# Optimization experiments

Hardware: AMD Instinct MI355X
Metric: run time of the kernel (lower is better)

Reference implementation:

```python
import jax, jax.numpy as jnp
import numpy as np

SEQ, BATCH, D_IN, D_HID, D_OUT = 2048, 256, 512, 512, 1000


def setup_inputs() -> dict:
    key = jax.random.key(0)
    ks = jax.random.split(key, 15)
    s_in = 1.0 / np.sqrt(D_IN)
    s_h = 1.0 / np.sqrt(D_HID)
    def lin(k, fan_in, shape, scale):
        return jax.random.uniform(k, shape, jnp.float32, -scale, scale)
    return {
        "x": jax.random.normal(ks[0], (SEQ, BATCH, D_IN), jnp.float32),
        # weights stored as [in, out] so y = x @ W + b
        "Wz": lin(ks[1], D_IN, (D_IN, D_HID), s_in),  "bz": lin(ks[2], D_IN, (D_HID,), s_in),
        "Uz": lin(ks[3], D_HID, (D_HID, D_HID), s_h), "buz": lin(ks[4], D_HID, (D_HID,), s_h),
        "Wr": lin(ks[5], D_IN, (D_IN, D_HID), s_in),  "br": lin(ks[6], D_IN, (D_HID,), s_in),
        "Ur": lin(ks[7], D_HID, (D_HID, D_HID), s_h), "bur": lin(ks[8], D_HID, (D_HID,), s_h),
        "Wh": lin(ks[9], D_IN, (D_IN, D_HID), s_in),  "bh": lin(ks[10], D_IN, (D_HID,), s_in),
        "Uh": lin(ks[11], D_HID, (D_HID, D_HID), s_h), "buh": lin(ks[12], D_HID, (D_HID,), s_h),
        "Wfc": lin(ks[13], D_HID, (D_HID, D_OUT), s_h), "bfc": lin(ks[14], D_HID, (D_OUT,), s_h),
    }


def reference(x, Wz, bz, Uz, buz, Wr, br, Ur, bur, Wh, bh, Uh, buh, Wfc, bfc):
    B, H = x.shape[1], Uz.shape[0]

    def gru_step(h, xt):
        # xt: [B, D_IN], h: [B, H]
        z = jax.nn.sigmoid(xt @ Wz + bz + h @ Uz + buz)
        r = jax.nn.sigmoid(xt @ Wr + br + h @ Ur + bur)
        h_tild = jnp.tanh(xt @ Wh + bh + (r * h) @ Uh + buh)
        h_new = (1.0 - z) * h + z * h_tild
        return h_new, None

    h0 = jnp.zeros((B, H), x.dtype)  # zero init hidden (broadcast-equivalent)
    h, _ = jax.lax.scan(gru_step, h0, x)
    out = jax.nn.relu(h) @ Wfc + bfc        # [B, D_OUT]
    out = out[None]                          # [1, B, D_OUT]
    return jax.nn.log_softmax(out, axis=1)  # dim=1 as in torch module
```

## Files before the change

kernel.cpp:

```cpp
#include <hip/hip_runtime.h>


typedef unsigned short ushort_t;
typedef unsigned int uint_t;
typedef __bf16 bf16_t;
typedef bf16_t bf16x8 __attribute__((ext_vector_type(8)));
typedef float f32x4 __attribute__((ext_vector_type(4)));
typedef uint_t u32x4 __attribute__((ext_vector_type(4)));

__device__ __forceinline__ ushort_t f2bf(float f) {
  uint_t u = __float_as_uint(f);
  u += 0x7FFFu + ((u >> 16) & 1u);
  return (ushort_t)(u >> 16);
}
__device__ __forceinline__ float bfu2f(uint_t h) { return __uint_as_float(h << 16); }

__device__ __forceinline__ uint_t atom_add_ret(uint_t* p, uint_t v) {
  uint_t old;
  asm volatile("global_atomic_add %0, %1, %2, off sc0\n\t"
               "s_waitcnt vmcnt(0)"
               : "=v"(old) : "v"(p), "v"(v) : "memory");
  return old;
}
__device__ __forceinline__ void atom_add_noret(uint_t* p, uint_t v) {
  asm volatile("global_atomic_add %0, %1, off" :: "v"(p), "v"(v) : "memory");
}

__global__ __launch_bounds__(256) void prep_kernel(
    const float* __restrict__ Wz, const float* __restrict__ Wr, const float* __restrict__ Wh,
    const float* __restrict__ Uz, const float* __restrict__ Ur, const float* __restrict__ Uh,
    const float* __restrict__ bz, const float* __restrict__ buz,
    const float* __restrict__ br, const float* __restrict__ bur,
    const float* __restrict__ bh, const float* __restrict__ buh,
    ushort_t* __restrict__ UT, ushort_t* __restrict__ WT, float* __restrict__ gbias)
{
  const int idx = blockIdx.x * 256 + threadIdx.x;
  {
    const int gate = idx >> 18, n = (idx >> 9) & 511, k = idx & 511;
    const float* U = (gate == 0) ? Uz : (gate == 1 ? Ur : Uh);
    UT[idx] = f2bf(U[k * 512 + n]);
  }
  {
    const int n = idx >> 9, k = idx & 511;
    const int gate = n >> 9, nn = n & 511;
    const float* W = (gate == 0) ? Wz : (gate == 1 ? Wr : Wh);
    WT[idx] = f2bf(W[k * 512 + nn]);
  }
  if (idx < 1536) {
    const int gate = idx >> 9, nn = idx & 511;
    gbias[idx] = (gate == 0) ? (bz[nn] + buz[nn])
               : (gate == 1) ? (br[nn] + bur[nn])
                             : (bh[nn] + buh[nn]);
  }
}

__global__ __launch_bounds__(256) void gate_gemm(
    const float* __restrict__ x,
    const ushort_t* __restrict__ WT,
    const float* __restrict__ gbias,
    ushort_t* __restrict__ gout,
    int mtiles)
{
  __shared__ ushort_t A_sh[128 * 72];
  __shared__ ushort_t B_sh[128 * 72];
  const int bid = blockIdx.x;
  int mt, nt;
  if ((mtiles & 31) == 0) {
    const int sb = bid / 384;
    const int r = bid - sb * 384;
    mt = sb * 32 + (r & 31);
    nt = r >> 5;
  } else {
    mt = bid / 12;
    nt = bid - mt * 12;
  }
  const int mrow0 = mt * 128;
  const int ncol0 = nt * 128;
  const int tid = threadIdx.x;
  const int wid = tid >> 6;
  const int lane = tid & 63;
  const int wm = wid >> 1, wn = wid & 1;
  const int l15 = lane & 15, l4 = lane >> 4;

  const f32x4 vzero = {0.f, 0.f, 0.f, 0.f};
  f32x4 acc[4][4];
#pragma unroll
  for (int m = 0; m < 4; ++m)
#pragma unroll
    for (int n = 0; n < 4; ++n) acc[m][n] = vzero;

  const int ar = tid >> 4, ak = tid & 15;
  const int bn = tid >> 3, bk = tid & 7;

  for (int ks = 0; ks < 8; ++ks) {
    if (ks) __syncthreads();
    const int k0 = ks * 64;
#pragma unroll
    for (int p = 0; p < 8; ++p) {
      const int r = p * 16 + ar;
      const float4 v = *(const float4*)&x[(size_t)(mrow0 + r) * 512 + (k0 + ak * 4)];
      ushort4 hv;
      hv.x = f2bf(v.x); hv.y = f2bf(v.y); hv.z = f2bf(v.z); hv.w = f2bf(v.w);
      *(ushort4*)&A_sh[r * 72 + ak * 4] = hv;
    }
#pragma unroll
    for (int p = 0; p < 4; ++p) {
      const int n = p * 32 + bn;
      *(uint4*)&B_sh[n * 72 + bk * 8] =
          *(const uint4*)&WT[(size_t)(ncol0 + n) * 512 + (k0 + bk * 8)];
    }
    __syncthreads();
#pragma unroll
    for (int kk = 0; kk < 2; ++kk) {
      bf16x8 a[4], b[4];
#pragma unroll
      for (int m = 0; m < 4; ++m)
        a[m] = *(const bf16x8*)&A_sh[(wm * 64 + m * 16 + l15) * 72 + kk * 32 + l4 * 8];
#pragma unroll
      for (int n = 0; n < 4; ++n)
        b[n] = *(const bf16x8*)&B_sh[(wn * 64 + n * 16 + l15) * 72 + kk * 32 + l4 * 8];
#pragma unroll
      for (int m = 0; m < 4; ++m)
#pragma unroll
        for (int n = 0; n < 4; ++n)
          acc[m][n] = __builtin_amdgcn_mfma_f32_16x16x32_bf16(a[m], b[n], acc[m][n], 0, 0, 0);
    }
  }
#pragma unroll
  for (int n = 0; n < 4; ++n) {
    const int gcol = ncol0 + wn * 64 + n * 16 + l15;
    const float bv = gbias[gcol];
#pragma unroll
    for (int m = 0; m < 4; ++m) {
      const int grow = mrow0 + wm * 64 + m * 16 + l4 * 4;
#pragma unroll
      for (int q = 0; q < 4; ++q)
        gout[(size_t)(grow + q) * 1536 + gcol] = f2bf(acc[m][n][q] + bv);
    }
  }
}

__device__ __forceinline__ bool flag_barrier(uint_t* gflags, int j, int lane, int wid, int tid,
                                             uint_t nbar, int* s_dead) {
  asm volatile("s_waitcnt vmcnt(0)" ::: "memory");
  __syncthreads();
  if (tid == 0) atom_add_noret(gflags + j * 16, 1u);
  if (wid == 0) {
    int cnt = 0;
    for (;;) {
      uint_t v = nbar;
      if (lane < 16) v = atom_add_ret(gflags + lane * 16, 0u);
      if (!__any(v < nbar)) break;
      if (++cnt > (1 << 15)) { *s_dead = 1; break; }
    }
  }
  __syncthreads();
  return *s_dead != 0;
}

__device__ __forceinline__ void stage16x512(const ushort_t* __restrict__ src, int g,
                                            ushort_t* dst_lds, int tid) {
  const ushort_t* p[4];
#pragma unroll
  for (int k = 0; k < 4; ++k) {
    const int idx = tid + (k << 8);
    const int r = idx >> 6, kc = idx & 63;
    p[k] = src + (((g * 16 + r) << 9) + kc * 8);
  }
  u32x4 v0, v1, v2, v3;
  asm volatile(
      "global_load_dwordx4 %0, %4, off sc0\n\t"
      "global_load_dwordx4 %1, %5, off sc0\n\t"
      "global_load_dwordx4 %2, %6, off sc0\n\t"
      "global_load_dwordx4 %3, %7, off sc0\n\t"
      "s_waitcnt vmcnt(0)"
      : "=&v"(v0), "=&v"(v1), "=&v"(v2), "=&v"(v3)
      : "v"(p[0]), "v"(p[1]), "v"(p[2]), "v"(p[3])
      : "memory");
#pragma unroll
  for (int k = 0; k < 4; ++k) {
    const int idx = tid + (k << 8);
    const int r = idx >> 6, kc = idx & 63;
    *(u32x4*)&dst_lds[r * 520 + kc * 8] = (k == 0) ? v0 : (k == 1) ? v1 : (k == 2) ? v2 : v3;
  }
}

__global__ __launch_bounds__(256, 1) void gru_rec(
    const ushort_t* __restrict__ UT,
    const ushort_t* __restrict__ gates,
    ushort_t* __restrict__ h_buf,
    ushort_t* __restrict__ rh_buf,
    float* __restrict__ h_state,
    uint_t* __restrict__ bars,
    int Tc, int first)
{
  __shared__ ushort_t h_st[16 * 520];
  __shared__ float z_sh[512];
  __shared__ float hown[512];
  __shared__ float red[512];
  __shared__ int s_dead;

  const int tid = threadIdx.x;
  const int bid = blockIdx.x;
  const int g = bid & 15;
  const int j = bid >> 4;
  const int wid = tid >> 6;
  const int lane = tid & 63;
  const int l15 = lane & 15;
  const int l4 = lane >> 4;
  if (tid == 0) s_dead = 0;

  uint_t* gflags = bars + g * 256;
  uint_t nbar = 0;

  const int p1gate = wid >> 1;
  const int p1nt = wid & 1;
  const int p2nt = wid >> 1;
  const int p2kh = wid & 1;

  bf16x8 UB[16];
  {
    const size_t base = (size_t)((p1gate << 9) + j * 32 + p1nt * 16 + l15) * 512 + (size_t)(l4 * 8);
#pragma unroll
    for (int kk = 0; kk < 16; ++kk) UB[kk] = *(const bf16x8*)&UT[base + (size_t)kk * 32];
  }
  bf16x8 UH[8];
  {
    const size_t base = (size_t)(1024 + j * 32 + p2nt * 16 + l15) * 512 + (size_t)(p2kh * 256 + l4 * 8);
#pragma unroll
    for (int kk = 0; kk < 8; ++kk) UH[kk] = *(const bf16x8*)&UT[base + (size_t)kk * 32];
  }

  if (first) {
    for (int i = tid; i < 512; i += 256) {
      const int r = i >> 5, c = i & 31;
      h_buf[((g * 16 + r) << 9) + j * 32 + c] = 0;
      hown[i] = 0.f;
    }
  } else {
    for (int i = tid; i < 512; i += 256) {
      const int r = i >> 5, c = i & 31;
      hown[i] = h_state[((g * 16 + r) << 9) + j * 32 + c];
    }
  }
  ++nbar;
  if (flag_barrier(gflags, j, lane, wid, tid, nbar, &s_dead)) return;

  const int colg1 = j * 32 + p1nt * 16 + l15;
  const int colg2 = j * 32 + p2nt * 16 + l15;

  uint_t c1u[4], c2u[4], n1u[4], n2u[4];
  {
    const size_t gb = (size_t)(g * 16) * 1536;
#pragma unroll
    for (int q = 0; q < 4; ++q) {
      n1u[q] = gates[gb + (size_t)(l4 * 4 + q) * 1536 + (p1gate << 9) + colg1];
      n2u[q] = gates[gb + (size_t)(l4 * 4 + q) * 1536 + 1024 + colg2];
    }
  }

  for (int tt = 0; tt < Tc; ++tt) {
    stage16x512(h_buf, g, h_st, tid);
    __syncthreads();
#pragma unroll
    for (int q = 0; q < 4; ++q) { c1u[q] = n1u[q]; c2u[q] = n2u[q]; }
    {
      const ushort_t* ap = &h_st[l15 * 520 + l4 * 8];
      f32x4 a0 = {0.f, 0.f, 0.f, 0.f}, a1 = {0.f, 0.f, 0.f, 0.f};
#pragma unroll
      for (int kk = 0; kk < 16; kk += 2) {
        a0 = __builtin_amdgcn_mfma_f32_16x16x32_bf16(*(const bf16x8*)(ap + kk * 32), UB[kk], a0, 0, 0, 0);
        a1 = __builtin_amdgcn_mfma_f32_16x16x32_bf16(*(const bf16x8*)(ap + kk * 32 + 32), UB[kk + 1], a1, 0, 0, 0);
      }
      const f32x4 acc = a0 + a1;
      const int lc = p1nt * 16 + l15;
#pragma unroll
      for (int q = 0; q < 4; ++q) {
        const int row = l4 * 4 + q;
        const float pre = acc[q] + bfu2f(c1u[q]);
        const float s = 1.f / (1.f + __expf(-pre));
        if (p1gate == 0) z_sh[row * 32 + lc] = s;
        else rh_buf[((g * 16 + row) << 9) + j * 32 + lc] = f2bf(s * hown[row * 32 + lc]);
      }
    }
    ++nbar;
    if (flag_barrier(gflags, j, lane, wid, tid, nbar, &s_dead)) break;

    stage16x512(rh_buf, g, h_st, tid);
    __syncthreads();
    if (tt + 1 < Tc) {
      const size_t gb = (size_t)((size_t)(tt + 1) * 256 + g * 16) * 1536;
#pragma unroll
      for (int q = 0; q < 4; ++q) {
        n1u[q] = gates[gb + (size_t)(l4 * 4 + q) * 1536 + (p1gate << 9) + colg1];
        n2u[q] = gates[gb + (size_t)(l4 * 4 + q) * 1536 + 1024 + colg2];
      }
    }
    {
      const ushort_t* ap = &h_st[l15 * 520 + p2kh * 256 + l4 * 8];
      f32x4 a0 = {0.f, 0.f, 0.f, 0.f}, a1 = {0.f, 0.f, 0.f, 0.f};
#pragma unroll
      for (int kk = 0; kk < 8; kk += 2) {
        a0 = __builtin_amdgcn_mfma_f32_16x16x32_bf16(*(const bf16x8*)(ap + kk * 32), UH[kk], a0, 0, 0, 0);
        a1 = __builtin_amdgcn_mfma_f32_16x16x32_bf16(*(const bf16x8*)(ap + kk * 32 + 32), UH[kk + 1], a1, 0, 0, 0);
      }
      const f32x4 acc = a0 + a1;
      if (p2kh == 1) {
#pragma unroll
        for (int q = 0; q < 4; ++q) red[p2nt * 256 + (l4 * 4 + q) * 16 + l15] = acc[q];
      }
      __syncthreads();
      if (p2kh == 0) {
        const int lc = p2nt * 16 + l15;
#pragma unroll
        for (int q = 0; q < 4; ++q) {
          const int row = l4 * 4 + q;
          const float dot = acc[q] + red[p2nt * 256 + row * 16 + l15];
          float pre = dot + bfu2f(c2u[q]);
          pre = fminf(15.f, fmaxf(-15.f, pre));
          const float e = __expf(2.f * pre);
          const float th = (e - 1.f) / (e + 1.f);
          const float z = z_sh[row * 32 + lc];
          const float hold = hown[row * 32 + lc];
          const float hnew = (1.f - z) * hold + z * th;
          hown[row * 32 + lc] = hnew;
          h_buf[((g * 16 + row) << 9) + j * 32 + lc] = f2bf(hnew);
          if (tt == Tc - 1) h_state[((g * 16 + row) << 9) + j * 32 + lc] = hnew;
        }
      }
    }
    ++nbar;
    if (flag_barrier(gflags, j, lane, wid, tid, nbar, &s_dead)) break;
  }
}

__global__ __launch_bounds__(256) void fc_kernel(
    const float* __restrict__ h, const float* __restrict__ Wfc,
    const float* __restrict__ bfc, float* __restrict__ logits)
{
  __shared__ float hsh[16][520];
  const int tid = threadIdx.x;
  const int by = blockIdx.y;
  {
    const int r = tid >> 4, seg = tid & 15;
    const float* src = &h[(size_t)(by * 16 + r) * 512 + seg * 32];
#pragma unroll
    for (int i = 0; i < 8; ++i) {
      float4 v = *(const float4*)&src[i * 4];
      v.x = fmaxf(v.x, 0.f); v.y = fmaxf(v.y, 0.f);
      v.z = fmaxf(v.z, 0.f); v.w = fmaxf(v.w, 0.f);
      *(float4*)&hsh[r][seg * 32 + i * 4] = v;
    }
  }
  __syncthreads();
  const int c = tid & 63, rq = tid >> 6;
  const int gc = blockIdx.x * 64 + c;
  if (gc >= 1000) return;
  float acc0 = 0.f, acc1 = 0.f, acc2 = 0.f, acc3 = 0.f;
  for (int k = 0; k < 512; ++k) {
    const float w = Wfc[(size_t)k * 1000 + gc];
    acc0 += hsh[rq * 4 + 0][k] * w;
    acc1 += hsh[rq * 4 + 1][k] * w;
    acc2 += hsh[rq * 4 + 2][k] * w;
    acc3 += hsh[rq * 4 + 3][k] * w;
  }
  const float bv = bfc[gc];
  const int r0 = by * 16 + rq * 4;
  logits[(size_t)(r0 + 0) * 1000 + gc] = acc0 + bv;
  logits[(size_t)(r0 + 1) * 1000 + gc] = acc1 + bv;
  logits[(size_t)(r0 + 2) * 1000 + gc] = acc2 + bv;
  logits[(size_t)(r0 + 3) * 1000 + gc] = acc3 + bv;
}

__global__ __launch_bounds__(256) void lsm_kernel(const float* __restrict__ logits,
                                                  float* __restrict__ out)
{
  const int c = blockIdx.x, tid = threadIdx.x;
  const int wid = tid >> 6, lane = tid & 63;
  __shared__ float red[8];
  const float v = logits[(size_t)tid * 1000 + c];
  float m = v;
#pragma unroll
  for (int o = 32; o >= 1; o >>= 1) m = fmaxf(m, __shfl_xor(m, o));
  if (lane == 0) red[wid] = m;
  __syncthreads();
  m = fmaxf(fmaxf(red[0], red[1]), fmaxf(red[2], red[3]));
  float s = __expf(v - m);
#pragma unroll
  for (int o = 32; o >= 1; o >>= 1) s += __shfl_xor(s, o);
  if (lane == 0) red[4 + wid] = s;
  __syncthreads();
  s = red[4] + red[5] + red[6] + red[7];
  out[(size_t)tid * 1000 + c] = (v - m) - __logf(s);
}

extern "C" void kernel_launch(void* const* d_in, const int* in_sizes, int n_in,
                              void* d_out, int out_size, void* d_ws, size_t ws_size,
                              hipStream_t stream) {
  (void)in_sizes; (void)n_in; (void)out_size;
  const float* x   = (const float*)d_in[0];
  const float* Wz  = (const float*)d_in[1];
  const float* bz  = (const float*)d_in[2];
  const float* Uz  = (const float*)d_in[3];
  const float* buz = (const float*)d_in[4];
  const float* Wr  = (const float*)d_in[5];
  const float* br  = (const float*)d_in[6];
  const float* Ur  = (const float*)d_in[7];
  const float* bur = (const float*)d_in[8];
  const float* Wh  = (const float*)d_in[9];
  const float* bh  = (const float*)d_in[10];
  const float* Uh  = (const float*)d_in[11];
  const float* buh = (const float*)d_in[12];
  const float* Wfc = (const float*)d_in[13];
  const float* bfc = (const float*)d_in[14];
  float* out = (float*)d_out;
  char* ws = (char*)d_ws;

  ushort_t* UT     = (ushort_t*)(ws + 0);
  ushort_t* WT     = (ushort_t*)(ws + 1572864);
  float*    gbias  = (float*)(ws + 3145728);
  ushort_t* h_buf  = (ushort_t*)(ws + 3151872);
  ushort_t* rh_buf = (ushort_t*)(ws + 3414016);
  float*    hstate = (float*)(ws + 3676160);
  float*    logits = (float*)(ws + 4200448);
  uint_t*   bars   = (uint_t*)(ws + 5224448);
  ushort_t* gates  = (ushort_t*)(ws + 5240832);

  const size_t fixed = 5240832;
  const size_t per_step = (size_t)256 * 1536 * 2;
  int Tc_max = 2048;
  if (ws_size < fixed + (size_t)2048 * per_step) {
    const size_t avail = (ws_size > fixed) ? (ws_size - fixed) : 0;
    Tc_max = (int)(avail / per_step);
    Tc_max &= ~15;
    if (Tc_max < 16) Tc_max = 16;
  }

  prep_kernel<<<3072, 256, 0, stream>>>(Wz, Wr, Wh, Uz, Ur, Uh,
                                        bz, buz, br, bur, bh, buh, UT, WT, gbias);

  int done = 0;
  while (done < 2048) {
    const int Tc = (2048 - done < Tc_max) ? (2048 - done) : Tc_max;
    const int mtiles = Tc * 2;
    gate_gemm<<<mtiles * 12, 256, 0, stream>>>(x + (size_t)done * 256 * 512, WT, gbias, gates, mtiles);
    hipMemsetAsync(bars, 0, 16384, stream);
    gru_rec<<<256, 256, 0, stream>>>(UT, gates, h_buf, rh_buf, hstate, bars, Tc, done == 0 ? 1 : 0);
    done += Tc;
  }
  fc_kernel<<<dim3(16, 16), 256, 0, stream>>>(hstate, Wfc, bfc, logits);
  lsm_kernel<<<1000, 256, 0, stream>>>(logits, out);
}
```

Baseline: 10.90 ms.

## Interleave two batch sub-groups per block with counter-based split barriers

The recurrent kernel now runs on 128 blocks, each owning two 16-row batch groups (A and B). Phases for the two groups are interleaved so that while one group waits on its barrier, the other group's work can proceed. The per-block flag array with all-lane polling is replaced by a single shared arrival counter per group, polled by one thread with s_sleep. This is meant to hide inter-block synchronisation latency and cut polling traffic, at the cost of half as many blocks and more serial work per block.

```diff
diff --git a/kernel.cpp b/kernel.cpp
--- a/kernel.cpp
+++ b/kernel.cpp
@@ -140,32 +140,14 @@
   }
 }
 
-__device__ __forceinline__ bool flag_barrier(uint_t* gflags, int j, int lane, int wid, int tid,
-                                             uint_t nbar, int* s_dead) {
-  asm volatile("s_waitcnt vmcnt(0)" ::: "memory");
-  __syncthreads();
-  if (tid == 0) atom_add_noret(gflags + j * 16, 1u);
-  if (wid == 0) {
-    int cnt = 0;
-    for (;;) {
-      uint_t v = nbar;
-      if (lane < 16) v = atom_add_ret(gflags + lane * 16, 0u);
-      if (!__any(v < nbar)) break;
-      if (++cnt > (1 << 15)) { *s_dead = 1; break; }
-    }
-  }
-  __syncthreads();
-  return *s_dead != 0;
-}
-
-__device__ __forceinline__ void stage16x512(const ushort_t* __restrict__ src, int g,
+__device__ __forceinline__ void stage16x512(const ushort_t* __restrict__ src,
                                             ushort_t* dst_lds, int tid) {
   const ushort_t* p[4];
 #pragma unroll
   for (int k = 0; k < 4; ++k) {
     const int idx = tid + (k << 8);
     const int r = idx >> 6, kc = idx & 63;
-    p[k] = src + (((g * 16 + r) << 9) + kc * 8);
+    p[k] = src + ((r << 9) + kc * 8);
   }
   u32x4 v0, v1, v2, v3;
   asm volatile(
@@ -195,23 +177,25 @@
     int Tc, int first)
 {
   __shared__ ushort_t h_st[16 * 520];
-  __shared__ float z_sh[512];
-  __shared__ float hown[512];
+  __shared__ float z_shA[512], z_shB[512];
+  __shared__ float hownA[512], hownB[512];
   __shared__ float red[512];
   __shared__ int s_dead;
 
   const int tid = threadIdx.x;
   const int bid = blockIdx.x;
-  const int g = bid & 15;
-  const int j = bid >> 4;
+  const int p = bid & 7;
+  const int j = bid >> 3;
   const int wid = tid >> 6;
   const int lane = tid & 63;
   const int l15 = lane & 15;
   const int l4 = lane >> 4;
   if (tid == 0) s_dead = 0;
 
-  uint_t* gflags = bars + g * 256;
-  uint_t nbar = 0;
+  const int row0A = p * 32;
+  const int row0B = p * 32 + 16;
+  uint_t* ctrA = bars + p * 32;
+  uint_t* ctrB = bars + p * 32 + 16;
 
   const int p1gate = wid >> 1;
   const int p1nt = wid & 1;
@@ -234,104 +218,142 @@
   if (first) {
     for (int i = tid; i < 512; i += 256) {
       const int r = i >> 5, c = i & 31;
-      h_buf[((g * 16 + r) << 9) + j * 32 + c] = 0;
-      hown[i] = 0.f;
+      h_buf[((size_t)(row0A + r) << 9) + j * 32 + c] = 0;
+      h_buf[((size_t)(row0B + r) << 9) + j * 32 + c] = 0;
+      hownA[i] = 0.f;
+      hownB[i] = 0.f;
     }
   } else {
     for (int i = tid; i < 512; i += 256) {
       const int r = i >> 5, c = i & 31;
-      hown[i] = h_state[((g * 16 + r) << 9) + j * 32 + c];
-    }
-  }
-  ++nbar;
-  if (flag_barrier(gflags, j, lane, wid, tid, nbar, &s_dead)) return;
-
-  const int colg1 = j * 32 + p1nt * 16 + l15;
-  const int colg2 = j * 32 + p2nt * 16 + l15;
-
-  uint_t c1u[4], c2u[4], n1u[4], n2u[4];
-  {
-    const size_t gb = (size_t)(g * 16) * 1536;
+      hownA[i] = h_state[((size_t)(row0A + r) << 9) + j * 32 + c];
+      hownB[i] = h_state[((size_t)(row0B + r) << 9) + j * 32 + c];
+    }
+  }
+  asm volatile("s_waitcnt vmcnt(0)" ::: "memory");
+  __syncthreads();
+  if (tid == 0) { atom_add_noret(ctrA, 1u); atom_add_noret(ctrB, 1u); }
+  uint_t tgtA = 16, tgtB = 16;
+
+  const int colg1 = (p1gate << 9) + j * 32 + p1nt * 16 + l15;
+  const int colg2 = 1024 + j * 32 + p2nt * 16 + l15;
+
+  uint_t n1uA[4], n2uA[4], n1uB[4], n2uB[4];
+  {
+    const size_t gbA = (size_t)(row0A + l4 * 4) * 1536;
+    const size_t gbB = (size_t)(row0B + l4 * 4) * 1536;
 #pragma unroll
     for (int q = 0; q < 4; ++q) {
-      n1u[q] = gates[gb + (size_t)(l4 * 4 + q) * 1536 + (p1gate << 9) + colg1];
-      n2u[q] = gates[gb + (size_t)(l4 * 4 + q) * 1536 + 1024 + colg2];
-    }
-  }
+      n1uA[q] = gates[gbA + (size_t)q * 1536 + colg1];
+      n2uA[q] = gates[gbA + (size_t)q * 1536 + colg2];
+      n1uB[q] = gates[gbB + (size_t)q * 1536 + colg1];
+      n2uB[q] = gates[gbB + (size_t)q * 1536 + colg2];
+    }
+  }
+
+#define POLL(ctr, tgt)                                              \
+  if (tid == 0) {                                                   \
+    int cnt_ = 0;                                                   \
+    for (;;) {                                                      \
+      const uint_t seen_ = atom_add_ret(ctr, 0u);                   \
+      if (seen_ >= (tgt)) break;                                    \
+      __builtin_amdgcn_s_sleep(1);                                  \
+      if (++cnt_ > (1 << 15)) { s_dead = 1; break; }                \
+    }                                                               \
+  }                                                                 \
+  __syncthreads();                                                  \
+  if (s_dead) break;
+
+#define ARRIVE(ctr, tgt)                                            \
+  asm volatile("s_waitcnt vmcnt(0)" ::: "memory");                  \
+  __syncthreads();                                                  \
+  if (tid == 0) atom_add_noret(ctr, 1u);                            \
+  (tgt) += 16;
+
+#define PHASE1(S)                                                              \
+  POLL(ctr##S, tgt##S);                                                        \
+  stage16x512(h_buf + ((size_t)row0##S << 9), h_st, tid);                      \
+  __syncthreads();                                                             \
+  {                                                                            \
+    const ushort_t* ap = &h_st[l15 * 520 + l4 * 8];                            \
+    f32x4 a0 = {0.f, 0.f, 0.f, 0.f}, a1 = {0.f, 0.f, 0.f, 0.f};                \
+    _Pragma("unroll")                                                          \
+    for (int kk = 0; kk < 16; kk += 2) {                                       \
+      a0 = __builtin_amdgcn_mfma_f32_16x16x32_bf16(*(const bf16x8*)(ap + kk * 32), UB[kk], a0, 0, 0, 0); \
+      a1 = __builtin_amdgcn_mfma_f32_16x16x32_bf16(*(const bf16x8*)(ap + kk * 32 + 32), UB[kk + 1], a1, 0, 0, 0); \
+    }                                                                          \
+    const f32x4 acc = a0 + a1;                                                 \
+    const int lc = p1nt * 16 + l15;                                            \
+    _Pragma("unroll")                                                          \
+    for (int q = 0; q < 4; ++q) {                                              \
+      const int row = l4 * 4 + q;                                              \
+      const float pre = acc[q] + bfu2f(n1u##S[q]);                             \
+      const float s = 1.f / (1.f + __expf(-pre));                              \
+      if (p1gate == 0) z_sh##S[row * 32 + lc] = s;                             \
+      else rh_buf[((size_t)(row0##S + row) << 9) + j * 32 + lc] =              \
+               f2bf(s * hown##S[row * 32 + lc]);                               \
+    }                                                                          \
+  }                                                                            \
+  ARRIVE(ctr##S, tgt##S);
+
+#define PHASE2(S)                                                              \
+  POLL(ctr##S, tgt##S);                                                        \
+  stage16x512(rh_buf + ((size_t)row0##S << 9), h_st, tid);                     \
+  __syncthreads();                                                             \
+  {                                                                            \
+    uint_t c2_[4] = {n2u##S[0], n2u##S[1], n2u##S[2], n2u##S[3]};              \
+    if (tt + 1 < Tc) {                                                         \
+      const size_t gb = ((size_t)(tt + 1) * 256 + row0##S + l4 * 4) * 1536;    \
+      _Pragma("unroll")                                                        \
+      for (int q = 0; q < 4; ++q) {                                            \
+        n1u##S[q] = gates[gb + (size_t)q * 1536 + colg1];                      \
+        n2u##S[q] = gates[gb + (size_t)q * 1536 + colg2];                      \
+      }                                                                        \
+    }                                                                          \
+    const ushort_t* ap = &h_st[l15 * 520 + p2kh * 256 + l4 * 8];               \
+    f32x4 a0 = {0.f, 0.f, 0.f, 0.f}, a1 = {0.f, 0.f, 0.f, 0.f};                \
+    _Pragma("unroll")                                                          \
+    for (int kk = 0; kk < 8; kk += 2) {                                        \
+      a0 = __builtin_amdgcn_mfma_f32_16x16x32_bf16(*(const bf16x8*)(ap + kk * 32), UH[kk], a0, 0, 0, 0); \
+      a1 = __builtin_amdgcn_mfma_f32_16x16x32_bf16(*(const bf16x8*)(ap + kk * 32 + 32), UH[kk + 1], a1, 0, 0, 0); \
+    }                                                                          \
+    const f32x4 acc = a0 + a1;                                                 \
+    if (p2kh == 1) {                                                           \
+      _Pragma("unroll")                                                        \
+      for (int q = 0; q < 4; ++q) red[p2nt * 256 + (l4 * 4 + q) * 16 + l15] = acc[q]; \
+    }                                                                          \
+    __syncthreads();                                                           \
+    if (p2kh == 0) {                                                           \
+      const int lc = p2nt * 16 + l15;                                          \
+      _Pragma("unroll")                                                        \
+      for (int q = 0; q < 4; ++q) {                                            \
+        const int row = l4 * 4 + q;                                            \
+        const float dot = acc[q] + red[p2nt * 256 + row * 16 + l15];           \
+        float pre = dot + bfu2f(c2_[q]);                                       \
+        pre = fminf(15.f, fmaxf(-15.f, pre));                                  \
+        const float e = __expf(2.f * pre);                                     \
+        const float th = (e - 1.f) / (e + 1.f);                                \
+        const float z = z_sh##S[row * 32 + lc];                                \
+        const float hold = hown##S[row * 32 + lc];                             \
+        const float hnew = (1.f - z) * hold + z * th;                          \
+        hown##S[row * 32 + lc] = hnew;                                         \
+        h_buf[((size_t)(row0##S + row) << 9) + j * 32 + lc] = f2bf(hnew);      \
+        if (tt == Tc - 1) h_state[((size_t)(row0##S + row) << 9) + j * 32 + lc] = hnew; \
+      }                                                                        \
+    }                                                                          \
+  }                                                                            \
+  ARRIVE(ctr##S, tgt##S);
 
   for (int tt = 0; tt < Tc; ++tt) {
-    stage16x512(h_buf, g, h_st, tid);
-    __syncthreads();
-#pragma unroll
-    for (int q = 0; q < 4; ++q) { c1u[q] = n1u[q]; c2u[q] = n2u[q]; }
-    {
-      const ushort_t* ap = &h_st[l15 * 520 + l4 * 8];
-      f32x4 a0 = {0.f, 0.f, 0.f, 0.f}, a1 = {0.f, 0.f, 0.f, 0.f};
-#pragma unroll
-      for (int kk = 0; kk < 16; kk += 2) {
-        a0 = __builtin_amdgcn_mfma_f32_16x16x32_bf16(*(const bf16x8*)(ap + kk * 32), UB[kk], a0, 0, 0, 0);
-        a1 = __builtin_amdgcn_mfma_f32_16x16x32_bf16(*(const bf16x8*)(ap + kk * 32 + 32), UB[kk + 1], a1, 0, 0, 0);
-      }
-      const f32x4 acc = a0 + a1;
-      const int lc = p1nt * 16 + l15;
-#pragma unroll
-      for (int q = 0; q < 4; ++q) {
-        const int row = l4 * 4 + q;
-        const float pre = acc[q] + bfu2f(c1u[q]);
-        const float s = 1.f / (1.f + __expf(-pre));
-        if (p1gate == 0) z_sh[row * 32 + lc] = s;
-        else rh_buf[((g * 16 + row) << 9) + j * 32 + lc] = f2bf(s * hown[row * 32 + lc]);
-      }
-    }
-    ++nbar;
-    if (flag_barrier(gflags, j, lane, wid, tid, nbar, &s_dead)) break;
-
-    stage16x512(rh_buf, g, h_st, tid);
-    __syncthreads();
-    if (tt + 1 < Tc) {
-      const size_t gb = (size_t)((size_t)(tt + 1) * 256 + g * 16) * 1536;
-#pragma unroll
-      for (int q = 0; q < 4; ++q) {
-        n1u[q] = gates[gb + (size_t)(l4 * 4 + q) * 1536 + (p1gate << 9) + colg1];
-        n2u[q] = gates[gb + (size_t)(l4 * 4 + q) * 1536 + 1024 + colg2];
-      }
-    }
-    {
-      const ushort_t* ap = &h_st[l15 * 520 + p2kh * 256 + l4 * 8];
-      f32x4 a0 = {0.f, 0.f, 0.f, 0.f}, a1 = {0.f, 0.f, 0.f, 0.f};
-#pragma unroll
-      for (int kk = 0; kk < 8; kk += 2) {
-        a0 = __builtin_amdgcn_mfma_f32_16x16x32_bf16(*(const bf16x8*)(ap + kk * 32), UH[kk], a0, 0, 0, 0);
-        a1 = __builtin_amdgcn_mfma_f32_16x16x32_bf16(*(const bf16x8*)(ap + kk * 32 + 32), UH[kk + 1], a1, 0, 0, 0);
-      }
-      const f32x4 acc = a0 + a1;
-      if (p2kh == 1) {
-#pragma unroll
-        for (int q = 0; q < 4; ++q) red[p2nt * 256 + (l4 * 4 + q) * 16 + l15] = acc[q];
-      }
-      __syncthreads();
-      if (p2kh == 0) {
-        const int lc = p2nt * 16 + l15;
-#pragma unroll
-        for (int q = 0; q < 4; ++q) {
-          const int row = l4 * 4 + q;
-          const float dot = acc[q] + red[p2nt * 256 + row * 16 + l15];
-          float pre = dot + bfu2f(c2u[q]);
-          pre = fminf(15.f, fmaxf(-15.f, pre));
-          const float e = __expf(2.f * pre);
-          const float th = (e - 1.f) / (e + 1.f);
-          const float z = z_sh[row * 32 + lc];
-          const float hold = hown[row * 32 + lc];
-          const float hnew = (1.f - z) * hold + z * th;
-          hown[row * 32 + lc] = hnew;
-          h_buf[((g * 16 + row) << 9) + j * 32 + lc] = f2bf(hnew);
-          if (tt == Tc - 1) h_state[((g * 16 + row) << 9) + j * 32 + lc] = hnew;
-        }
-      }
-    }
-    ++nbar;
-    if (flag_barrier(gflags, j, lane, wid, tid, nbar, &s_dead)) break;
-  }
+    PHASE1(A);
+    PHASE1(B);
+    PHASE2(A);
+    PHASE2(B);
+  }
+#undef POLL
+#undef ARRIVE
+#undef PHASE1
+#undef PHASE2
 }
 
 __global__ __launch_bounds__(256) void fc_kernel(
@@ -424,9 +446,9 @@
   float*    hstate = (float*)(ws + 3676160);
   float*    logits = (float*)(ws + 4200448);
   uint_t*   bars   = (uint_t*)(ws + 5224448);
-  ushort_t* gates  = (ushort_t*)(ws + 5240832);
-
-  const size_t fixed = 5240832;
+  ushort_t* gates  = (ushort_t*)(ws + 5228544);
+
+  const size_t fixed = 5228544;
   const size_t per_step = (size_t)256 * 1536 * 2;
   int Tc_max = 2048;
   if (ws_size < fixed + (size_t)2048 * per_step) {
@@ -444,8 +466,8 @@
     const int Tc = (2048 - done < Tc_max) ? (2048 - done) : Tc_max;
     const int mtiles = Tc * 2;
     gate_gemm<<<mtiles * 12, 256, 0, stream>>>(x + (size_t)done * 256 * 512, WT, gbias, gates, mtiles);
-    hipMemsetAsync(bars, 0, 16384, stream);
-    gru_rec<<<256, 256, 0, stream>>>(UT, gates, h_buf, rh_buf, hstate, bars, Tc, done == 0 ? 1 : 0);
+    hipMemsetAsync(bars, 0, 4096, stream);
+    gru_rec<<<128, 256, 0, stream>>>(UT, gates, h_buf, rh_buf, hstate, bars, Tc, done == 0 ? 1 : 0);
     done += Tc;
   }
   fc_kernel<<<dim3(16, 16), 256, 0, stream>>>(hstate, Wfc, bfc, logits);
```

After: 15.46 ms. 41.9% more time.

## Replace per-block flag barrier with shared counter barrier and stagger h staging

Applied to the files above, without the earlier changes.

The group barrier changes from one flag per block, where a whole wave polls 16 flags, to a single atomic counter per group of 16 blocks, polled by one thread with s_sleep backoff. Staging loads are rotated by block index j so that blocks in a group start reading different rows of h/rh, spreading memory traffic. Contention on a single counter may grow, and the sleep can add wake-up latency to each of the three barriers per timestep.

```diff
diff --git a/kernel.cpp b/kernel.cpp
--- a/kernel.cpp
+++ b/kernel.cpp
@@ -140,17 +140,16 @@
   }
 }
 
-__device__ __forceinline__ bool flag_barrier(uint_t* gflags, int j, int lane, int wid, int tid,
-                                             uint_t nbar, int* s_dead) {
+__device__ __forceinline__ bool group_barrier(uint_t* ctr, uint_t target, int tid, int* s_dead) {
   asm volatile("s_waitcnt vmcnt(0)" ::: "memory");
   __syncthreads();
-  if (tid == 0) atom_add_noret(gflags + j * 16, 1u);
-  if (wid == 0) {
+  if (tid == 0) {
+    atom_add_noret(ctr, 1u);
     int cnt = 0;
     for (;;) {
-      uint_t v = nbar;
-      if (lane < 16) v = atom_add_ret(gflags + lane * 16, 0u);
-      if (!__any(v < nbar)) break;
+      const uint_t seen = atom_add_ret(ctr, 0u);
+      if (seen >= target) break;
+      __builtin_amdgcn_s_sleep(1);
       if (++cnt > (1 << 15)) { *s_dead = 1; break; }
     }
   }
@@ -158,12 +157,14 @@
   return *s_dead != 0;
 }
 
-__device__ __forceinline__ void stage16x512(const ushort_t* __restrict__ src, int g,
+__device__ __forceinline__ void stage16x512(const ushort_t* __restrict__ src, int g, int j,
                                             ushort_t* dst_lds, int tid) {
   const ushort_t* p[4];
+  int ridx[4];
 #pragma unroll
   for (int k = 0; k < 4; ++k) {
-    const int idx = tid + (k << 8);
+    const int idx = (tid + (k << 8) + j * 64) & 1023;
+    ridx[k] = idx;
     const int r = idx >> 6, kc = idx & 63;
     p[k] = src + (((g * 16 + r) << 9) + kc * 8);
   }
@@ -179,8 +180,7 @@
       : "memory");
 #pragma unroll
   for (int k = 0; k < 4; ++k) {
-    const int idx = tid + (k << 8);
-    const int r = idx >> 6, kc = idx & 63;
+    const int r = ridx[k] >> 6, kc = ridx[k] & 63;
     *(u32x4*)&dst_lds[r * 520 + kc * 8] = (k == 0) ? v0 : (k == 1) ? v1 : (k == 2) ? v2 : v3;
   }
 }
@@ -210,7 +210,7 @@
   const int l4 = lane >> 4;
   if (tid == 0) s_dead = 0;
 
-  uint_t* gflags = bars + g * 256;
+  uint_t* ctr = bars + g * 64;
   uint_t nbar = 0;
 
   const int p1gate = wid >> 1;
@@ -243,8 +243,7 @@
       hown[i] = h_state[((g * 16 + r) << 9) + j * 32 + c];
     }
   }
-  ++nbar;
-  if (flag_barrier(gflags, j, lane, wid, tid, nbar, &s_dead)) return;
+  if (group_barrier(ctr, (++nbar) * 16, tid, &s_dead)) return;
 
   const int colg1 = j * 32 + p1nt * 16 + l15;
   const int colg2 = j * 32 + p2nt * 16 + l15;
@@ -260,7 +259,7 @@
   }
 
   for (int tt = 0; tt < Tc; ++tt) {
-    stage16x512(h_buf, g, h_st, tid);
+    stage16x512(h_buf, g, j, h_st, tid);
     __syncthreads();
 #pragma unroll
     for (int q = 0; q < 4; ++q) { c1u[q] = n1u[q]; c2u[q] = n2u[q]; }
@@ -283,10 +282,9 @@
         else rh_buf[((g * 16 + row) << 9) + j * 32 + lc] = f2bf(s * hown[row * 32 + lc]);
       }
     }
-    ++nbar;
-    if (flag_barrier(gflags, j, lane, wid, tid, nbar, &s_dead)) break;
-
-    stage16x512(rh_buf, g, h_st, tid);
+    if (group_barrier(ctr, (++nbar) * 16, tid, &s_dead)) break;
+
+    stage16x512(rh_buf, g, j, h_st, tid);
     __syncthreads();
     if (tt + 1 < Tc) {
       const size_t gb = (size_t)((size_t)(tt + 1) * 256 + g * 16) * 1536;
@@ -329,8 +327,7 @@
         }
       }
     }
-    ++nbar;
-    if (flag_barrier(gflags, j, lane, wid, tid, nbar, &s_dead)) break;
+    if (group_barrier(ctr, (++nbar) * 16, tid, &s_dead)) break;
   }
 }
 
@@ -424,9 +421,9 @@
   float*    hstate = (float*)(ws + 3676160);
   float*    logits = (float*)(ws + 4200448);
   uint_t*   bars   = (uint_t*)(ws + 5224448);
-  ushort_t* gates  = (ushort_t*)(ws + 5240832);
-
-  const size_t fixed = 5240832;
+  ushort_t* gates  = (ushort_t*)(ws + 5228544);
+
+  const size_t fixed = 5228544;
   const size_t per_step = (size_t)256 * 1536 * 2;
   int Tc_max = 2048;
   if (ws_size < fixed + (size_t)2048 * per_step) {
@@ -444,7 +441,7 @@
     const int Tc = (2048 - done < Tc_max) ? (2048 - done) : Tc_max;
     const int mtiles = Tc * 2;
     gate_gemm<<<mtiles * 12, 256, 0, stream>>>(x + (size_t)done * 256 * 512, WT, gbias, gates, mtiles);
-    hipMemsetAsync(bars, 0, 16384, stream);
+    hipMemsetAsync(bars, 0, 4096, stream);
     gru_rec<<<256, 256, 0, stream>>>(UT, gates, h_buf, rh_buf, hstate, bars, Tc, done == 0 ? 1 : 0);
     done += Tc;
   }
```

Result: faster. 9.924 ms (-8.9%).
